# Kernel tuning notes

Hardware: AMD Instinct MI355X
Metric: run time of the kernel (lower is better)

Reference implementation:

```python
import jax, jax.numpy as jnp
import numpy as np

NEG_SLOPE = 0.2
EPS = 1e-16  # matches PyG-style segment softmax denominator guard

N_NODES = 50000
N_EDGES = 800000
IN_CH = 256
HEADS = 4
OUT_CH = 32


def setup_inputs() -> dict:
    key = jax.random.key(0)
    k1, k2, k3, k4 = jax.random.split(key, 4)
    nodes_ft = jax.random.normal(k1, (N_NODES, IN_CH), dtype=jnp.float32)
    adj_list = jax.random.randint(k2, (2, N_EDGES), 0, N_NODES, dtype=jnp.int64)
    # xavier-normal-ish scales
    weight = jax.random.normal(k3, (IN_CH, HEADS * OUT_CH), dtype=jnp.float32) * (
        (2.0 / (IN_CH + HEADS * OUT_CH)) ** 0.5
    )
    att = jax.random.normal(k4, (1, HEADS, 2 * OUT_CH), dtype=jnp.float32) * (
        (2.0 / (1 + 2 * OUT_CH)) ** 0.5
    )
    bias = jnp.zeros((HEADS * OUT_CH,), dtype=jnp.float32)
    return {"nodes_ft": nodes_ft, "adj_list": adj_list, "weight": weight, "att": att, "bias": bias}


def reference(nodes_ft, adj_list, weight, att, bias):
    N = nodes_ft.shape[0]
    H, C = att.shape[1], att.shape[2] // 2
    dst = adj_list[0]  # softmax / aggregation key
    src = adj_list[1]
    # node hidden states: [N, H, C]
    h = (nodes_ft @ weight).reshape(N, H, C)
    xi = h[dst]  # [E, H, C]
    xj = h[src]  # [E, H, C]
    # attention logits: cat([xi, xj]) . att  ==  xi.att_i + xj.att_j
    att_i, att_j = att[:, :, :C], att[:, :, C:]
    alpha = (xi * att_i).sum(-1) + (xj * att_j).sum(-1)  # [E, H]
    alpha = jax.nn.leaky_relu(alpha, negative_slope=NEG_SLOPE)
    # segment softmax over destination node
    m = jax.ops.segment_max(alpha, dst, num_segments=N)  # [N, H]
    m = jnp.where(jnp.isfinite(m), m, 0.0)
    e = jnp.exp(alpha - m[dst])
    s = jax.ops.segment_sum(e, dst, num_segments=N)  # [N, H]
    a = e / (s[dst] + EPS)  # [E, H]
    # weighted scatter-add aggregate
    vals = xj * a[:, :, None]  # [E, H, C]
    out = jax.ops.segment_sum(vals, dst, num_segments=N)  # [N, H, C]
    out = out.reshape(N, H * C) + bias  # concat=True
    return out
```

## Files before the change

### kernel.cpp

```cpp
#include <hip/hip_runtime.h>
#include <hip/hip_bf16.h>
#include <math.h>

#define NN 50000
#define NE 800000
#define IN_CH 256
#define HEADS 4
#define OUT_CH 32
#define HC 128
#define NEG_SLOPE 0.2f
#define GAT_EPS 1e-16f

#define SBS 1024
#define NB  ((NN + SBS - 1) / SBS)

#define NBINS 64
#define BINSH 10
#define NBBIN 49
#define NBLK  625
#define EPB   1280

#define OFF_HB     0
#define OFF_WT     (NN*HC/2)
#define OFF_AI     (OFF_WT + 16384)
#define OFF_AJ     (OFF_AI + NN*HEADS)
#define OFF_ROW    (OFF_AJ + NN*HEADS)
#define OFF_CUR    (OFF_ROW + NN + 4)
#define OFF_HIST   (OFF_CUR + NN + 4)
#define OFF_BSUM   (OFF_HIST + NN + 4)
#define OFF_BOFF   (OFF_BSUM + NB + 4)
#define OFF_BLKC   (OFF_BOFF + NB + 4)
#define OFF_BLKO   (OFF_BLKC + NBLK*NBINS)
#define OFF_PAIR   ((OFF_BLKO + NBLK*NBINS + 1) & ~1)
#define OFF_ESRC   (OFF_PAIR + 2*NE)

typedef __attribute__((ext_vector_type(8))) short short8v;
typedef __attribute__((ext_vector_type(4))) float float4v;

__device__ __forceinline__ unsigned short f2bf(float x) {
    union { float f; unsigned u; } v; v.f = x;
    unsigned r = v.u + 0x7fffu + ((v.u >> 16) & 1u);
    return (unsigned short)(r >> 16);
}
__device__ __forceinline__ float bf2f(unsigned short b) {
    union { unsigned u; float f; } v; v.u = ((unsigned)b) << 16;
    return v.f;
}

__global__ void k_zero(int* __restrict__ hist) {
    int i = blockIdx.x * blockDim.x + threadIdx.x;
    if (i < NN) hist[i] = 0;
}

__global__ void k_wt(const float* __restrict__ W, unsigned short* __restrict__ Wt) {
    int idx = blockIdx.x * blockDim.x + threadIdx.x;
    if (idx >= HC * IN_CH) return;
    int n = idx >> 8, k = idx & 255;
    Wt[n * IN_CH + k] = f2bf(W[(size_t)k * HC + n]);
}

__global__ __launch_bounds__(256) void k_gemm(const float* __restrict__ A,
                                              const unsigned short* __restrict__ Wt,
                                              unsigned short* __restrict__ Hb) {
    const int tid  = threadIdx.x;
    const int lane = tid & 63;
    const int w    = tid >> 6;
    const int wr   = w >> 1, wc = w & 1;
    const int blockRow = blockIdx.x * 128;

    const int lrow = lane & 15;
    const int kgrp = lane >> 4;

    float4v acc[4][4];
#pragma unroll
    for (int i = 0; i < 4; i++)
#pragma unroll
        for (int j = 0; j < 4; j++) acc[i][j] = (float4v){0.f, 0.f, 0.f, 0.f};

#pragma unroll
    for (int ks = 0; ks < 8; ks++) {
        const int kb = ks * 32 + kgrp * 8;
        short8v af[4], bfr[4];
#pragma unroll
        for (int mi = 0; mi < 4; mi++) {
            int r = blockRow + wr * 64 + mi * 16 + lrow;
            if (r >= NN) r = NN - 1;
            const float* ap = A + (size_t)r * IN_CH + kb;
            float4 a0 = *(const float4*)ap;
            float4 a1 = *(const float4*)(ap + 4);
            short8v t;
            t[0] = (short)f2bf(a0.x); t[1] = (short)f2bf(a0.y);
            t[2] = (short)f2bf(a0.z); t[3] = (short)f2bf(a0.w);
            t[4] = (short)f2bf(a1.x); t[5] = (short)f2bf(a1.y);
            t[6] = (short)f2bf(a1.z); t[7] = (short)f2bf(a1.w);
            af[mi] = t;
        }
#pragma unroll
        for (int ni = 0; ni < 4; ni++) {
            int c = wc * 64 + ni * 16 + lrow;
            bfr[ni] = *(const short8v*)(Wt + (size_t)c * IN_CH + kb);
        }
#pragma unroll
        for (int mi = 0; mi < 4; mi++)
#pragma unroll
            for (int ni = 0; ni < 4; ni++)
                acc[mi][ni] = __builtin_amdgcn_mfma_f32_16x16x32_bf16(
                    af[mi], bfr[ni], acc[mi][ni], 0, 0, 0);
    }

#pragma unroll
    for (int mi = 0; mi < 4; mi++) {
#pragma unroll
        for (int reg = 0; reg < 4; reg++) {
            int r = blockRow + wr * 64 + mi * 16 + kgrp * 4 + reg;
            if (r >= NN) continue;
#pragma unroll
            for (int ni = 0; ni < 4; ni++) {
                int c = wc * 64 + ni * 16 + lrow;
                Hb[(size_t)r * HC + c] = f2bf(acc[mi][ni][reg]);
            }
        }
    }
}

__global__ void k_att(const unsigned short* __restrict__ Hb, const float* __restrict__ att,
                      float* __restrict__ ai, float* __restrict__ aj) {
    int idx = blockIdx.x * blockDim.x + threadIdx.x;
    if (idx >= NN * HEADS) return;
    int n = idx >> 2, hh = idx & 3;
    const unsigned* hp = (const unsigned*)(Hb + (size_t)n * HC + hh * OUT_CH);
    const float* ati = att + hh * 2 * OUT_CH;
    const float* atj = ati + OUT_CH;
    float si = 0.f, sj = 0.f;
#pragma unroll
    for (int i = 0; i < 16; i++) {
        unsigned u = hp[i];
        float lo = bf2f((unsigned short)(u & 0xffff));
        float hi = bf2f((unsigned short)(u >> 16));
        si = fmaf(lo, ati[2 * i], si);     si = fmaf(hi, ati[2 * i + 1], si);
        sj = fmaf(lo, atj[2 * i], sj);     sj = fmaf(hi, atj[2 * i + 1], sj);
    }
    ai[idx] = si;
    aj[idx] = sj;
}

__global__ __launch_bounds__(256) void s_count(const int* __restrict__ adj,
                                               int* __restrict__ hist,
                                               int* __restrict__ blkcnt) {
    __shared__ int lh[NBINS];
    int b = blockIdx.x, t = threadIdx.x;
    if (t < NBINS) lh[t] = 0;
    __syncthreads();
    int e0 = b * EPB;
#pragma unroll
    for (int i = 0; i < 5; i++) {
        int e = e0 + i * 256 + t;
        int dst = adj[e];
        atomicAdd(&hist[dst], 1);
        atomicAdd(&lh[dst >> BINSH], 1);
    }
    __syncthreads();
    if (t < NBINS) blkcnt[b * NBINS + t] = lh[t];
}

__global__ __launch_bounds__(640) void s_scanblk(const int* __restrict__ blkcnt,
                                                 int* __restrict__ blkoff) {
    int bin = blockIdx.x, t = threadIdx.x;
    int c = (t < NBLK) ? blkcnt[t * NBINS + bin] : 0;
    int lane = t & 63, w = t >> 6;
    int inc = c;
#pragma unroll
    for (int off = 1; off < 64; off <<= 1) {
        int u = __shfl_up(inc, off);
        if (lane >= off) inc += u;
    }
    __shared__ int wsum[10];
    if (lane == 63) wsum[w] = inc;
    __syncthreads();
    int wpre = 0;
    for (int i = 0; i < w; i++) wpre += wsum[i];
    if (t < NBLK) blkoff[t * NBINS + bin] = wpre + inc - c;
}

__global__ __launch_bounds__(256) void s_pairs(const int* __restrict__ adj,
                                               const int* __restrict__ rowp,
                                               const int* __restrict__ blkoff,
                                               int2* __restrict__ paired) {
    __shared__ int lh[NBINS];
    __shared__ int base[NBINS];
    int b = blockIdx.x, t = threadIdx.x;
    if (t < NBINS) {
        lh[t] = 0;
        int n0 = t << BINSH;
        base[t] = rowp[n0 < NN ? n0 : NN] + blkoff[b * NBINS + t];
    }
    __syncthreads();
    int e0 = b * EPB;
#pragma unroll
    for (int i = 0; i < 5; i++) {
        int e = e0 + i * 256 + t;
        int dst = adj[e];
        int src = adj[NE + e];
        int bin = dst >> BINSH;
        int r = atomicAdd(&lh[bin], 1);
        paired[base[bin] + r] = make_int2(dst, src);
    }
}

__global__ __launch_bounds__(256) void s_csr(const int2* __restrict__ paired,
                                             const int* __restrict__ rowp,
                                             int* __restrict__ esrc) {
    __shared__ int cur2[1 << BINSH];
    int b = blockIdx.x, t = threadIdx.x;
    for (int i = t; i < (1 << BINSH); i += 256) cur2[i] = 0;
    __syncthreads();
    int n0 = b << BINSH;
    int n1 = n0 + (1 << BINSH); if (n1 > NN) n1 = NN;
    int e0 = rowp[n0], e1 = rowp[n1];
    for (int i = e0 + t; i < e1; i += 256) {
        int2 p = paired[i];
        int off = atomicAdd(&cur2[p.x - n0], 1);
        esrc[rowp[p.x] + off] = p.y;
    }
}

__global__ __launch_bounds__(256) void k_bsum(const int* __restrict__ hist,
                                              int* __restrict__ bsum) {
    int b = blockIdx.x, t = threadIdx.x;
    int i0 = b * SBS + t * 4;
    int s = 0;
#pragma unroll
    for (int j = 0; j < 4; j++) {
        int i = i0 + j;
        if (i < NN) s += hist[i];
    }
#pragma unroll
    for (int off = 32; off; off >>= 1) s += __shfl_xor(s, off);
    __shared__ int ws[4];
    int lane = t & 63, wid = t >> 6;
    if (lane == 0) ws[wid] = s;
    __syncthreads();
    if (t == 0) bsum[b] = ws[0] + ws[1] + ws[2] + ws[3];
}

__global__ __launch_bounds__(64) void k_bscan(const int* __restrict__ bsum,
                                              int* __restrict__ boff) {
    int lane = threadIdx.x;
    int v = (lane < NB) ? bsum[lane] : 0;
    int inc = v;
#pragma unroll
    for (int off = 1; off < 64; off <<= 1) {
        int u = __shfl_up(inc, off);
        if (lane >= off) inc += u;
    }
    if (lane < NB) boff[lane] = inc - v;
}

__global__ __launch_bounds__(256) void k_bwrite(const int* __restrict__ hist,
                                                const int* __restrict__ boff,
                                                int* __restrict__ row,
                                                int* __restrict__ cur) {
    int b = blockIdx.x, t = threadIdx.x;
    int i0 = b * SBS + t * 4;
    int v[4];
    int s = 0;
#pragma unroll
    for (int j = 0; j < 4; j++) {
        int i = i0 + j;
        v[j] = (i < NN) ? hist[i] : 0;
        s += v[j];
    }
    int lane = t & 63, wid = t >> 6;
    int inc = s;
#pragma unroll
    for (int off = 1; off < 64; off <<= 1) {
        int u = __shfl_up(inc, off);
        if (lane >= off) inc += u;
    }
    __shared__ int wsum[4];
    if (lane == 63) wsum[wid] = inc;
    __syncthreads();
    int woff = 0;
    for (int w2 = 0; w2 < wid; w2++) woff += wsum[w2];
    int run = boff[b] + woff + (inc - s);
#pragma unroll
    for (int j = 0; j < 4; j++) {
        int i = i0 + j;
        if (i < NN) {
            row[i] = run;
            cur[i] = run;
            run += v[j];
        }
    }
    if (b == 0 && t == 0) row[NN] = NE;
}

__device__ __forceinline__ float lrelu(float x) {
    return x > 0.f ? x : NEG_SLOPE * x;
}

__global__ __launch_bounds__(256) void k_gather(const int* __restrict__ row,
                                                const int* __restrict__ esrc,
                                                const float* __restrict__ ai,
                                                const float* __restrict__ aj,
                                                const unsigned short* __restrict__ Hb,
                                                const float* __restrict__ bias,
                                                float* __restrict__ out) {
    int gid = blockIdx.x * blockDim.x + threadIdx.x;
    int nid = gid >> 6;
    int lane = gid & 63;
    if (nid >= NN) return;
    int r0 = row[nid];
    int deg = row[nid + 1] - r0;

    float4 aiv = *(const float4*)&ai[nid * 4];

    float mx0 = -INFINITY, mx1 = -INFINITY, mx2 = -INFINITY, mx3 = -INFINITY;
    for (int k = lane; k < deg; k += 64) {
        int s = esrc[r0 + k];
        float4 ajv = *(const float4*)&aj[s * 4];
        mx0 = fmaxf(mx0, lrelu(aiv.x + ajv.x));
        mx1 = fmaxf(mx1, lrelu(aiv.y + ajv.y));
        mx2 = fmaxf(mx2, lrelu(aiv.z + ajv.z));
        mx3 = fmaxf(mx3, lrelu(aiv.w + ajv.w));
    }
#pragma unroll
    for (int off = 32; off; off >>= 1) {
        mx0 = fmaxf(mx0, __shfl_xor(mx0, off));
        mx1 = fmaxf(mx1, __shfl_xor(mx1, off));
        mx2 = fmaxf(mx2, __shfl_xor(mx2, off));
        mx3 = fmaxf(mx3, __shfl_xor(mx3, off));
    }

    float s0 = 0.f, s1 = 0.f, s2 = 0.f, s3 = 0.f;
    for (int k = lane; k < deg; k += 64) {
        int s = esrc[r0 + k];
        float4 ajv = *(const float4*)&aj[s * 4];
        s0 += __expf(lrelu(aiv.x + ajv.x) - mx0);
        s1 += __expf(lrelu(aiv.y + ajv.y) - mx1);
        s2 += __expf(lrelu(aiv.z + ajv.z) - mx2);
        s3 += __expf(lrelu(aiv.w + ajv.w) - mx3);
    }
#pragma unroll
    for (int off = 32; off; off >>= 1) {
        s0 += __shfl_xor(s0, off);
        s1 += __shfl_xor(s1, off);
        s2 += __shfl_xor(s2, off);
        s3 += __shfl_xor(s3, off);
    }

    int c0 = lane * 2;
    int hh = lane >> 4;
    float mh  = (hh & 2) ? ((hh & 1) ? mx3 : mx2) : ((hh & 1) ? mx1 : mx0);
    float sh  = (hh & 2) ? ((hh & 1) ? s3 : s2) : ((hh & 1) ? s1 : s0);
    float aih = (hh & 2) ? ((hh & 1) ? aiv.w : aiv.z) : ((hh & 1) ? aiv.y : aiv.x);
    float inv = 1.0f / (sh + GAT_EPS);

    float accx = 0.f, accy = 0.f;
#pragma unroll 4
    for (int k = 0; k < deg; k++) {
        int s = esrc[r0 + k];
        float al = lrelu(aih + aj[s * 4 + hh]);
        float a = __expf(al - mh) * inv;
        unsigned hu = *(const unsigned*)(Hb + (size_t)s * HC + c0);
        accx = fmaf(bf2f((unsigned short)(hu & 0xffff)), a, accx);
        accy = fmaf(bf2f((unsigned short)(hu >> 16)), a, accy);
    }
    out[(size_t)nid * HC + c0]     = accx + bias[c0];
    out[(size_t)nid * HC + c0 + 1] = accy + bias[c0 + 1];
}

extern "C" void kernel_launch(void* const* d_in, const int* in_sizes, int n_in,
                              void* d_out, int out_size, void* d_ws, size_t ws_size,
                              hipStream_t stream) {
    const float* nodes  = (const float*)d_in[0];
    const int*   adj    = (const int*)d_in[1];
    const float* weight = (const float*)d_in[2];
    const float* att    = (const float*)d_in[3];
    const float* bias   = (const float*)d_in[4];
    float* out = (float*)d_out;
    float* ws  = (float*)d_ws;

    unsigned short* Hb = (unsigned short*)(ws + OFF_HB);
    unsigned short* Wt = (unsigned short*)(ws + OFF_WT);
    float* ai    = ws + OFF_AI;
    float* aj    = ws + OFF_AJ;
    int*   rowp  = (int*)(ws + OFF_ROW);
    int*   cur   = (int*)(ws + OFF_CUR);
    int*   hist  = (int*)(ws + OFF_HIST);
    int*   bsum  = (int*)(ws + OFF_BSUM);
    int*   boff  = (int*)(ws + OFF_BOFF);
    int*   blkc  = (int*)(ws + OFF_BLKC);
    int*   blko  = (int*)(ws + OFF_BLKO);
    int2*  pair  = (int2*)(ws + OFF_PAIR);
    int*   esrc  = (int*)(ws + OFF_ESRC);

    k_zero<<<(NN + 255) / 256, 256, 0, stream>>>(hist);
    s_count<<<NBLK, 256, 0, stream>>>(adj, hist, blkc);
    k_bsum<<<NB, 256, 0, stream>>>(hist, bsum);
    k_bscan<<<1, 64, 0, stream>>>(bsum, boff);
    k_bwrite<<<NB, 256, 0, stream>>>(hist, boff, rowp, cur);
    s_scanblk<<<NBINS, 640, 0, stream>>>(blkc, blko);
    s_pairs<<<NBLK, 256, 0, stream>>>(adj, rowp, blko, pair);
    s_csr<<<NBBIN, 256, 0, stream>>>(pair, rowp, esrc);
    k_wt<<<(HC * IN_CH + 255) / 256, 256, 0, stream>>>(weight, Wt);
    k_gemm<<<(NN + 127) / 128, 256, 0, stream>>>(nodes, Wt, Hb);
    k_att<<<(NN * HEADS + 255) / 256, 256, 0, stream>>>(Hb, att, ai, aj);
    k_gather<<<(NN * 64 + 255) / 256, 256, 0, stream>>>(rowp, esrc, ai, aj, Hb, bias, out);
}
```

Measured before the change: 275.2 us.

## Use online softmax, shuffle-broadcast edge weights in gather, merge init kernels

The gather kernel replaces the separate max and sum passes over incoming edges with a single online-softmax pass that rescales running sums and merges them across lanes with shuffles. The aggregation loop now has 16 lanes cooperatively load 16 edge indices and compute their attention weights, then broadcasts them with shuffles instead of every lane reloading esrc and aj and recomputing exp for each edge. The histogram zeroing and weight transpose are fused into one launch, removing a kernel launch. The cost is extra exp calls in the online softmax and shuffle overhead per edge.

```diff
diff --git a/kernel.cpp b/kernel.cpp
--- a/kernel.cpp
+++ b/kernel.cpp
@@ -10,6 +10,7 @@
 #define HC 128
 #define NEG_SLOPE 0.2f
 #define GAT_EPS 1e-16f
+#define NEG_BIG -1e30f
 
 #define SBS 1024
 #define NB  ((NN + SBS - 1) / SBS)
@@ -42,21 +43,23 @@
     unsigned r = v.u + 0x7fffu + ((v.u >> 16) & 1u);
     return (unsigned short)(r >> 16);
 }
-__device__ __forceinline__ float bf2f(unsigned short b) {
-    union { unsigned u; float f; } v; v.u = ((unsigned)b) << 16;
+__device__ __forceinline__ float bf2f_lo(unsigned u) {
+    union { unsigned u; float f; } v; v.u = u << 16;
     return v.f;
 }
-
-__global__ void k_zero(int* __restrict__ hist) {
-    int i = blockIdx.x * blockDim.x + threadIdx.x;
-    if (i < NN) hist[i] = 0;
-}
-
-__global__ void k_wt(const float* __restrict__ W, unsigned short* __restrict__ Wt) {
+__device__ __forceinline__ float bf2f_hi(unsigned u) {
+    union { unsigned u; float f; } v; v.u = u & 0xffff0000u;
+    return v.f;
+}
+
+__global__ void k_init(int* __restrict__ hist, const float* __restrict__ W,
+                       unsigned short* __restrict__ Wt) {
     int idx = blockIdx.x * blockDim.x + threadIdx.x;
-    if (idx >= HC * IN_CH) return;
-    int n = idx >> 8, k = idx & 255;
-    Wt[n * IN_CH + k] = f2bf(W[(size_t)k * HC + n]);
+    if (idx < NN) hist[idx] = 0;
+    if (idx < HC * IN_CH) {
+        int n = idx >> 8, k = idx & 255;
+        Wt[n * IN_CH + k] = f2bf(W[(size_t)k * HC + n]);
+    }
 }
 
 __global__ __launch_bounds__(256) void k_gemm(const float* __restrict__ A,
@@ -135,8 +138,8 @@
 #pragma unroll
     for (int i = 0; i < 16; i++) {
         unsigned u = hp[i];
-        float lo = bf2f((unsigned short)(u & 0xffff));
-        float hi = bf2f((unsigned short)(u >> 16));
+        float lo = bf2f_lo(u);
+        float hi = bf2f_hi(u);
         si = fmaf(lo, ati[2 * i], si);     si = fmaf(hi, ati[2 * i + 1], si);
         sj = fmaf(lo, atj[2 * i], sj);     sj = fmaf(hi, atj[2 * i + 1], sj);
     }
@@ -315,56 +318,59 @@
 
     float4 aiv = *(const float4*)&ai[nid * 4];
 
-    float mx0 = -INFINITY, mx1 = -INFINITY, mx2 = -INFINITY, mx3 = -INFINITY;
-    for (int k = lane; k < deg; k += 64) {
-        int s = esrc[r0 + k];
-        float4 ajv = *(const float4*)&aj[s * 4];
-        mx0 = fmaxf(mx0, lrelu(aiv.x + ajv.x));
-        mx1 = fmaxf(mx1, lrelu(aiv.y + ajv.y));
-        mx2 = fmaxf(mx2, lrelu(aiv.z + ajv.z));
-        mx3 = fmaxf(mx3, lrelu(aiv.w + ajv.w));
-    }
-#pragma unroll
-    for (int off = 32; off; off >>= 1) {
-        mx0 = fmaxf(mx0, __shfl_xor(mx0, off));
-        mx1 = fmaxf(mx1, __shfl_xor(mx1, off));
-        mx2 = fmaxf(mx2, __shfl_xor(mx2, off));
-        mx3 = fmaxf(mx3, __shfl_xor(mx3, off));
-    }
-
+    float m0 = NEG_BIG, m1 = NEG_BIG, m2 = NEG_BIG, m3 = NEG_BIG;
     float s0 = 0.f, s1 = 0.f, s2 = 0.f, s3 = 0.f;
     for (int k = lane; k < deg; k += 64) {
         int s = esrc[r0 + k];
         float4 ajv = *(const float4*)&aj[s * 4];
-        s0 += __expf(lrelu(aiv.x + ajv.x) - mx0);
-        s1 += __expf(lrelu(aiv.y + ajv.y) - mx1);
-        s2 += __expf(lrelu(aiv.z + ajv.z) - mx2);
-        s3 += __expf(lrelu(aiv.w + ajv.w) - mx3);
+        float a0 = lrelu(aiv.x + ajv.x);
+        float a1 = lrelu(aiv.y + ajv.y);
+        float a2 = lrelu(aiv.z + ajv.z);
+        float a3 = lrelu(aiv.w + ajv.w);
+        float n0 = fmaxf(m0, a0); s0 = s0 * __expf(m0 - n0) + __expf(a0 - n0); m0 = n0;
+        float n1 = fmaxf(m1, a1); s1 = s1 * __expf(m1 - n1) + __expf(a1 - n1); m1 = n1;
+        float n2 = fmaxf(m2, a2); s2 = s2 * __expf(m2 - n2) + __expf(a2 - n2); m2 = n2;
+        float n3 = fmaxf(m3, a3); s3 = s3 * __expf(m3 - n3) + __expf(a3 - n3); m3 = n3;
     }
 #pragma unroll
     for (int off = 32; off; off >>= 1) {
-        s0 += __shfl_xor(s0, off);
-        s1 += __shfl_xor(s1, off);
-        s2 += __shfl_xor(s2, off);
-        s3 += __shfl_xor(s3, off);
+        float om, os, nm;
+        om = __shfl_xor(m0, off); os = __shfl_xor(s0, off);
+        nm = fmaxf(m0, om); s0 = s0 * __expf(m0 - nm) + os * __expf(om - nm); m0 = nm;
+        om = __shfl_xor(m1, off); os = __shfl_xor(s1, off);
+        nm = fmaxf(m1, om); s1 = s1 * __expf(m1 - nm) + os * __expf(om - nm); m1 = nm;
+        om = __shfl_xor(m2, off); os = __shfl_xor(s2, off);
+        nm = fmaxf(m2, om); s2 = s2 * __expf(m2 - nm) + os * __expf(om - nm); m2 = nm;
+        om = __shfl_xor(m3, off); os = __shfl_xor(s3, off);
+        nm = fmaxf(m3, om); s3 = s3 * __expf(m3 - nm) + os * __expf(om - nm); m3 = nm;
     }
 
     int c0 = lane * 2;
     int hh = lane >> 4;
-    float mh  = (hh & 2) ? ((hh & 1) ? mx3 : mx2) : ((hh & 1) ? mx1 : mx0);
+    float mh  = (hh & 2) ? ((hh & 1) ? m3 : m2) : ((hh & 1) ? m1 : m0);
     float sh  = (hh & 2) ? ((hh & 1) ? s3 : s2) : ((hh & 1) ? s1 : s0);
     float aih = (hh & 2) ? ((hh & 1) ? aiv.w : aiv.z) : ((hh & 1) ? aiv.y : aiv.x);
     float inv = 1.0f / (sh + GAT_EPS);
 
     float accx = 0.f, accy = 0.f;
+    int ec = lane & 15;
+    for (int kc = 0; kc < deg; kc += 16) {
+        int nk = deg - kc; if (nk > 16) nk = 16;
+        int sv = 0; float av = 0.f;
+        if (ec < nk) {
+            sv = esrc[r0 + kc + ec];
+            float ajv = aj[sv * 4 + hh];
+            float al = lrelu(aih + ajv);
+            av = __expf(al - mh) * inv;
+        }
 #pragma unroll 4
-    for (int k = 0; k < deg; k++) {
-        int s = esrc[r0 + k];
-        float al = lrelu(aih + aj[s * 4 + hh]);
-        float a = __expf(al - mh) * inv;
-        unsigned hu = *(const unsigned*)(Hb + (size_t)s * HC + c0);
-        accx = fmaf(bf2f((unsigned short)(hu & 0xffff)), a, accx);
-        accy = fmaf(bf2f((unsigned short)(hu >> 16)), a, accy);
+        for (int k = 0; k < nk; k++) {
+            int s = __shfl(sv, k);
+            float a = __shfl(av, (hh << 4) | k);
+            unsigned hu = *(const unsigned*)(Hb + (size_t)s * HC + c0);
+            accx = fmaf(bf2f_lo(hu), a, accx);
+            accy = fmaf(bf2f_hi(hu), a, accy);
+        }
     }
     out[(size_t)nid * HC + c0]     = accx + bias[c0];
     out[(size_t)nid * HC + c0 + 1] = accy + bias[c0 + 1];
@@ -395,7 +401,7 @@
     int2*  pair  = (int2*)(ws + OFF_PAIR);
     int*   esrc  = (int*)(ws + OFF_ESRC);
 
-    k_zero<<<(NN + 255) / 256, 256, 0, stream>>>(hist);
+    k_init<<<(NN + 255) / 256, 256, 0, stream>>>(hist, weight, Wt);
     s_count<<<NBLK, 256, 0, stream>>>(adj, hist, blkc);
     k_bsum<<<NB, 256, 0, stream>>>(hist, bsum);
     k_bscan<<<1, 64, 0, stream>>>(bsum, boff);
@@ -403,7 +409,6 @@
     s_scanblk<<<NBINS, 640, 0, stream>>>(blkc, blko);
     s_pairs<<<NBLK, 256, 0, stream>>>(adj, rowp, blko, pair);
     s_csr<<<NBBIN, 256, 0, stream>>>(pair, rowp, esrc);
-    k_wt<<<(HC * IN_CH + 255) / 256, 256, 0, stream>>>(weight, Wt);
     k_gemm<<<(NN + 127) / 128, 256, 0, stream>>>(nodes, Wt, Hb);
     k_att<<<(NN * HEADS + 255) / 256, 256, 0, stream>>>(Hb, att, ai, aj);
     k_gather<<<(NN * 64 + 255) / 256, 256, 0, stream>>>(rowp, esrc, ai, aj, Hb, bias, out);
```

After: 290.6 us. 1.06x slower.
